# Optimization experiments

Hardware: AMD Instinct MI355X
Metric: run time of the kernel (lower is better)

## Reference

```python
import jax, jax.numpy as jnp
import numpy as np


def setup_inputs() -> dict:
    key = jax.random.key(0)
    k1, k2 = jax.random.split(key)
    B, S, D = 4, 8192, 1024
    x = jax.random.normal(k1, (B, S, D), dtype=jnp.float32)
    alpha = jax.random.uniform(k2, (B, S, D), dtype=jnp.float32)
    return {"x": x, "alpha": alpha}


def reference(x, alpha):
    # Linear recurrence h_t = alpha_t * h_{t-1} + x_t, computed as an
    # associative scan over the sequence axis (axis=1).
    def linear_combine(i, j):
        x_i, a_i = i
        x_j, a_j = j
        return (a_j * x_i + x_j, a_j * a_i)

    ys, _ = jax.lax.associative_scan(linear_combine, (x, alpha), axis=1)
    return ys
```

## Files before the change

kernel.cpp:

```cpp
#include <hip/hip_runtime.h>

constexpr int B  = 4;
constexpr int S  = 8192;
constexpr int D  = 1024;
constexpr int C  = 128;
constexpr int L  = S / C;
constexpr int D4 = D / 4;

__global__ __launch_bounds__(256) void phase1(const float4* __restrict__ x,
                                              const float4* __restrict__ a,
                                              float4* __restrict__ Xagg,
                                              float4* __restrict__ Aagg) {
    const int t = threadIdx.x;
    const int c = blockIdx.x;
    const int b = blockIdx.y;
    long base = ((long)(b * S + c * L)) * D4 + t;

    float4 X = {0.f, 0.f, 0.f, 0.f};
    float4 A = {1.f, 1.f, 1.f, 1.f};
    #pragma unroll 8
    for (int s = 0; s < L; ++s) {
        float4 xv = x[base + (long)s * D4];
        float4 av = a[base + (long)s * D4];
        X.x = fmaf(av.x, X.x, xv.x);
        X.y = fmaf(av.y, X.y, xv.y);
        X.z = fmaf(av.z, X.z, xv.z);
        X.w = fmaf(av.w, X.w, xv.w);
        A.x *= av.x; A.y *= av.y; A.z *= av.z; A.w *= av.w;
    }
    long o = ((long)(b * C + c)) * D4 + t;
    Xagg[o] = X;
    Aagg[o] = A;
}

__global__ __launch_bounds__(256) void phase2(float* __restrict__ Xagg,
                                              const float* __restrict__ Aagg) {
    const int g = blockIdx.x * blockDim.x + threadIdx.x;
    const int b = g / D;
    const int d = g % D;
    long base = (long)b * C * D + d;
    float carry = 0.f;
    for (int c = 0; c < C; ++c) {
        long o = base + (long)c * D;
        float X = Xagg[o];
        float A = Aagg[o];
        Xagg[o] = carry;
        carry = fmaf(A, carry, X);
    }
}

__global__ __launch_bounds__(256) void phase3(const float4* __restrict__ x,
                                              const float4* __restrict__ a,
                                              const float4* __restrict__ prefix,
                                              float4* __restrict__ out) {
    const int t = threadIdx.x;
    const int c = blockIdx.x;
    const int b = blockIdx.y;

    float4 h = prefix[((long)(b * C + c)) * D4 + t];
    long base = ((long)(b * S + c * L)) * D4 + t;
    #pragma unroll 8
    for (int s = 0; s < L; ++s) {
        float4 xv = x[base + (long)s * D4];
        float4 av = a[base + (long)s * D4];
        h.x = fmaf(av.x, h.x, xv.x);
        h.y = fmaf(av.y, h.y, xv.y);
        h.z = fmaf(av.z, h.z, xv.z);
        h.w = fmaf(av.w, h.w, xv.w);
        out[base + (long)s * D4] = h;
    }
}

extern "C" void kernel_launch(void* const* d_in, const int* in_sizes, int n_in,
                              void* d_out, int out_size, void* d_ws, size_t ws_size,
                              hipStream_t stream) {
    const float4* x = (const float4*)d_in[0];
    const float4* a = (const float4*)d_in[1];
    float4* out = (float4*)d_out;

    float* Xagg = (float*)d_ws;
    float* Aagg = Xagg + (size_t)B * C * D;

    dim3 grid1(C, B);
    phase1<<<grid1, 256, 0, stream>>>(x, a, (float4*)Xagg, (float4*)Aagg);

    phase2<<<(B * D) / 256, 256, 0, stream>>>(Xagg, Aagg);

    phase3<<<grid1, 256, 0, stream>>>(x, a, (const float4*)Xagg, out);
}
```

Baseline: 371.1 us.

## Raise chunk count to 512 when workspace allows and batch phase-2 loads

Templates the three-pass scan on the chunk count and picks 512 chunks when the workspace is large enough, falling back to 128 otherwise. This raises the grid of phases 1 and 3 from 512 to 2048 blocks, giving more waves to hide memory latency on a bandwidth-bound scan. Phase 2 now loads eight aggregates before running the serial carry chain, to overlap its dependent loads, but it has a longer chain of 512 steps. Unroll factors drop from 8 to 4.

```diff
diff --git a/kernel.cpp b/kernel.cpp
--- a/kernel.cpp
+++ b/kernel.cpp
@@ -3,72 +3,93 @@
 constexpr int B  = 4;
 constexpr int S  = 8192;
 constexpr int D  = 1024;
-constexpr int C  = 128;
-constexpr int L  = S / C;
 constexpr int D4 = D / 4;
 
-__global__ __launch_bounds__(256) void phase1(const float4* __restrict__ x,
-                                              const float4* __restrict__ a,
-                                              float4* __restrict__ Xagg,
-                                              float4* __restrict__ Aagg) {
+template <int C>
+__global__ __launch_bounds__(256) void phase1_k(const float4* __restrict__ x,
+                                                const float4* __restrict__ a,
+                                                float4* __restrict__ Xagg,
+                                                float4* __restrict__ Aagg) {
+    constexpr int L = S / C;
     const int t = threadIdx.x;
     const int c = blockIdx.x;
     const int b = blockIdx.y;
-    long base = ((long)(b * S + c * L)) * D4 + t;
+    size_t base = ((size_t)(b * S + c * L)) * D4 + t;
 
     float4 X = {0.f, 0.f, 0.f, 0.f};
     float4 A = {1.f, 1.f, 1.f, 1.f};
-    #pragma unroll 8
+    #pragma unroll 4
     for (int s = 0; s < L; ++s) {
-        float4 xv = x[base + (long)s * D4];
-        float4 av = a[base + (long)s * D4];
+        float4 xv = x[base + (size_t)s * D4];
+        float4 av = a[base + (size_t)s * D4];
         X.x = fmaf(av.x, X.x, xv.x);
         X.y = fmaf(av.y, X.y, xv.y);
         X.z = fmaf(av.z, X.z, xv.z);
         X.w = fmaf(av.w, X.w, xv.w);
         A.x *= av.x; A.y *= av.y; A.z *= av.z; A.w *= av.w;
     }
-    long o = ((long)(b * C + c)) * D4 + t;
+    size_t o = ((size_t)(b * C + c)) * D4 + t;
     Xagg[o] = X;
     Aagg[o] = A;
 }
 
-__global__ __launch_bounds__(256) void phase2(float* __restrict__ Xagg,
-                                              const float* __restrict__ Aagg) {
-    const int g = blockIdx.x * blockDim.x + threadIdx.x;
-    const int b = g / D;
-    const int d = g % D;
-    long base = (long)b * C * D + d;
-    float carry = 0.f;
-    for (int c = 0; c < C; ++c) {
-        long o = base + (long)c * D;
-        float X = Xagg[o];
-        float A = Aagg[o];
-        Xagg[o] = carry;
-        carry = fmaf(A, carry, X);
+template <int C>
+__global__ __launch_bounds__(256) void phase2_k(float* Xagg,
+                                                const float* __restrict__ Aagg) {
+    const int g = blockIdx.x * 256 + threadIdx.x;
+    const int b = g >> 10;
+    const int d = g & (D - 1);
+    const size_t base = (size_t)b * C * D + d;
+    constexpr int U = 8;
+    float xb[U], ab[U];
+    float h = 0.f;
+    for (int c0 = 0; c0 < C; c0 += U) {
+        #pragma unroll
+        for (int j = 0; j < U; ++j) {
+            xb[j] = Xagg[base + (size_t)(c0 + j) * D];
+            ab[j] = Aagg[base + (size_t)(c0 + j) * D];
+        }
+        #pragma unroll
+        for (int j = 0; j < U; ++j) {
+            Xagg[base + (size_t)(c0 + j) * D] = h;
+            h = fmaf(ab[j], h, xb[j]);
+        }
     }
 }
 
-__global__ __launch_bounds__(256) void phase3(const float4* __restrict__ x,
-                                              const float4* __restrict__ a,
-                                              const float4* __restrict__ prefix,
-                                              float4* __restrict__ out) {
+template <int C>
+__global__ __launch_bounds__(256) void phase3_k(const float4* __restrict__ x,
+                                                const float4* __restrict__ a,
+                                                const float4* __restrict__ prefix,
+                                                float4* __restrict__ out) {
+    constexpr int L = S / C;
     const int t = threadIdx.x;
     const int c = blockIdx.x;
     const int b = blockIdx.y;
 
-    float4 h = prefix[((long)(b * C + c)) * D4 + t];
-    long base = ((long)(b * S + c * L)) * D4 + t;
-    #pragma unroll 8
+    float4 h = prefix[((size_t)(b * C + c)) * D4 + t];
+    size_t base = ((size_t)(b * S + c * L)) * D4 + t;
+    #pragma unroll 4
     for (int s = 0; s < L; ++s) {
-        float4 xv = x[base + (long)s * D4];
-        float4 av = a[base + (long)s * D4];
+        float4 xv = x[base + (size_t)s * D4];
+        float4 av = a[base + (size_t)s * D4];
         h.x = fmaf(av.x, h.x, xv.x);
         h.y = fmaf(av.y, h.y, xv.y);
         h.z = fmaf(av.z, h.z, xv.z);
         h.w = fmaf(av.w, h.w, xv.w);
-        out[base + (long)s * D4] = h;
+        out[base + (size_t)s * D4] = h;
     }
+}
+
+template <int C>
+static void run_pipeline(const float4* x, const float4* a, float4* out,
+                         void* d_ws, hipStream_t stream) {
+    float* Xagg = (float*)d_ws;
+    float* Aagg = Xagg + (size_t)B * C * D;
+    dim3 grid1(C, B);
+    phase1_k<C><<<grid1, 256, 0, stream>>>(x, a, (float4*)Xagg, (float4*)Aagg);
+    phase2_k<C><<<(B * D) / 256, 256, 0, stream>>>(Xagg, Aagg);
+    phase3_k<C><<<grid1, 256, 0, stream>>>(x, a, (const float4*)Xagg, out);
 }
 
 extern "C" void kernel_launch(void* const* d_in, const int* in_sizes, int n_in,
@@ -78,13 +99,9 @@
     const float4* a = (const float4*)d_in[1];
     float4* out = (float4*)d_out;
 
-    float* Xagg = (float*)d_ws;
-    float* Aagg = Xagg + (size_t)B * C * D;
-
-    dim3 grid1(C, B);
-    phase1<<<grid1, 256, 0, stream>>>(x, a, (float4*)Xagg, (float4*)Aagg);
-
-    phase2<<<(B * D) / 256, 256, 0, stream>>>(Xagg, Aagg);
-
-    phase3<<<grid1, 256, 0, stream>>>(x, a, (const float4*)Xagg, out);
+    if (ws_size >= 2ull * B * 512 * D * sizeof(float)) {
+        run_pipeline<512>(x, a, out, d_ws, stream);
+    } else {
+        run_pipeline<128>(x, a, out, d_ws, stream);
+    }
 }
```

Result: slower. 398.9 us (+7.5%).
